# Kernel optimization log

Hardware: AMD Instinct MI355X
Metric: run time of the kernel (lower is better)

Reference implementation:

```python
import jax, jax.numpy as jnp
import numpy as np
from jax.ops import segment_sum

N_NODES = 100000
N_EDGES = 1600000
D = 128
N_LAYERS = 4
N_GRAPHS = 512
LN_EPS = 1e-5


def setup_inputs() -> dict:
    key = jax.random.key(0)
    ks = jax.random.split(key, 8)
    x = jax.random.normal(ks[0], (N_NODES, D), dtype=jnp.float32)
    edge_index = jax.random.randint(ks[1], (2, N_EDGES), 0, N_NODES, dtype=jnp.int64)
    batch = jnp.sort(jax.random.randint(ks[2], (N_NODES,), 0, N_GRAPHS, dtype=jnp.int64))
    scale = 1.0 / np.sqrt(D)
    Ws = jax.random.normal(ks[3], (N_LAYERS, D, D), dtype=jnp.float32) * scale
    bs = jnp.zeros((N_LAYERS, D), dtype=jnp.float32)
    gammas = jnp.ones((N_LAYERS, D), dtype=jnp.float32)
    betas = jnp.zeros((N_LAYERS, D), dtype=jnp.float32)
    lin_w = jax.random.normal(ks[4], (D, 1), dtype=jnp.float32) * scale
    lin_b = jnp.zeros((1,), dtype=jnp.float32)
    return {"x": x, "edge_index": edge_index, "batch": batch, "Ws": Ws,
            "bs": bs, "gammas": gammas, "betas": betas,
            "lin_w": lin_w, "lin_b": lin_b}


def _gcn_conv(x, W, b, src, dst, deg_inv_sqrt):
    # PyG GCNConv: h = x @ W, then sym-normalized aggregation over A + I, then + bias
    h = x @ W                                   # [N, D]
    coef = deg_inv_sqrt[src] * deg_inv_sqrt[dst]  # [E]
    msg = h[src] * coef[:, None]                # [E, D] gather (memory-bound)
    agg = segment_sum(msg, dst, num_segments=x.shape[0])  # scatter-add
    agg = agg + h * (deg_inv_sqrt * deg_inv_sqrt)[:, None]  # self-loop term
    return agg + b


def _layernorm(x, gamma, beta):
    mu = jnp.mean(x, axis=-1, keepdims=True)
    var = jnp.mean(jnp.square(x - mu), axis=-1, keepdims=True)
    return (x - mu) * jax.lax.rsqrt(var + LN_EPS) * gamma + beta


def reference(x, edge_index, batch, Ws, bs, gammas, betas, lin_w, lin_b):
    n = x.shape[0]
    src, dst = edge_index[0], edge_index[1]
    # degree with self-loops (GCNConv adds self loops by default)
    deg = segment_sum(jnp.ones_like(dst, dtype=x.dtype), dst, num_segments=n) + 1.0
    deg_inv_sqrt = jax.lax.rsqrt(deg)

    h = _gcn_conv(x, Ws[0], bs[0], src, dst, deg_inv_sqrt)
    h = _layernorm(h, gammas[0], betas[0])
    h = jax.nn.relu(h)  # dropout is identity in eval mode
    for i in range(1, N_LAYERS):
        h_prev = h
        h = _gcn_conv(h, Ws[i], bs[i], src, dst, deg_inv_sqrt)
        h = _layernorm(h, gammas[i], betas[i])
        h = h + h_prev
        if i < N_LAYERS - 1:
            h = jax.nn.relu(h)

    # global mean pool over graphs
    sums = segment_sum(h, batch, num_segments=N_GRAPHS)        # [G, D]
    cnts = segment_sum(jnp.ones((n,), h.dtype), batch, num_segments=N_GRAPHS)
    pooled = sums / jnp.maximum(cnts, 1.0)[:, None]
    return pooled @ lin_w + lin_b  # [G, 1]
```

## Files before the change

kernel.cpp:

```cpp
#include <hip/hip_runtime.h>
#include <hip/hip_bf16.h>


typedef __hip_bfloat162 bf2;
typedef __attribute__((ext_vector_type(8))) short short8;
typedef __attribute__((ext_vector_type(4))) float f32x4;

#define P1B 512
#define BSH 7
#define BMSK 127
#define MAXB 3072

__global__ __launch_bounds__(256) void k_pA(const int* __restrict__ dst,
                                            int* __restrict__ bh,
                                            const float* __restrict__ Ws,
                                            __hip_bfloat16* __restrict__ Wt,
                                            int* __restrict__ row_off,
                                            float* __restrict__ gsum,
                                            int E, int NB, int n, int G) {
    if (blockIdx.x >= P1B + 256) {
        for (int i = threadIdx.x; i < G; i += 256) gsum[i] = 0.f;
        if (threadIdx.x == 0) row_off[n] = E;
        return;
    }
    if (blockIdx.x >= P1B) {
        int i = (blockIdx.x - P1B) * 256 + threadIdx.x;
        int layer = i >> 14;
        int m = i & 16383;
        int j = m & 7;
        int l = (m >> 3) & 63;
        int ckb = m >> 9;
        int kb = ckb & 3;
        int c = ckb >> 2;
        int quad = l >> 4, lr = l & 15;
        int k = kb * 32 + quad * 8 + j;
        int col = c * 16 + lr;
        Wt[i] = __float2bfloat16(Ws[layer * 16384 + k * 128 + col]);
        return;
    }
    __shared__ int h[1024];
    const int tid = threadIdx.x;
    for (int i = tid; i < NB; i += 256) h[i] = 0;
    __syncthreads();
    const int per = (((E + P1B - 1) / P1B) + 3) & ~3;
    const int e0 = blockIdx.x * per, e1 = min(E, e0 + per);
    for (int base = e0 + tid * 4; base < e1; base += 1024) {
        if (base + 4 <= e1) {
            int4 d4 = *(const int4*)(dst + base);
            atomicAdd(&h[d4.x >> BSH], 1);
            atomicAdd(&h[d4.y >> BSH], 1);
            atomicAdd(&h[d4.z >> BSH], 1);
            atomicAdd(&h[d4.w >> BSH], 1);
        } else {
            for (int j = base; j < e1; j++) atomicAdd(&h[dst[j] >> BSH], 1);
        }
    }
    __syncthreads();
    int* out = bh + (size_t)blockIdx.x * NB;
    for (int i = tid; i < NB; i += 256) out[i] = h[i];
}

__global__ __launch_bounds__(256) void k_pB(int* __restrict__ bh,
                                            int* __restrict__ btot, int NB) {
    __shared__ int s[256];
    const int b = blockIdx.x, tid = threadIdx.x;
    int v0 = bh[(size_t)(2 * tid) * NB + b];
    int v1 = bh[(size_t)(2 * tid + 1) * NB + b];
    int tsum = v0 + v1;
    s[tid] = tsum;
    __syncthreads();
    for (int off = 1; off < 256; off <<= 1) {
        int t = (tid >= off) ? s[tid - off] : 0;
        __syncthreads();
        s[tid] += t;
        __syncthreads();
    }
    int excl = s[tid] - tsum;
    bh[(size_t)(2 * tid) * NB + b] = excl;
    bh[(size_t)(2 * tid + 1) * NB + b] = excl + v0;
    if (tid == 255) btot[b] = s[255];
}

__global__ __launch_bounds__(256) void k_pC(const int* __restrict__ src,
                                            const int* __restrict__ dst,
                                            const int* __restrict__ bh,
                                            const int* __restrict__ btot,
                                            int* __restrict__ bbase,
                                            unsigned* __restrict__ ebuf,
                                            int E, int NB) {
    __shared__ int cur[1024];
    __shared__ int s[256];
    const int tid = threadIdx.x;
    int v[4];
    int tsum = 0;
#pragma unroll
    for (int j = 0; j < 4; j++) {
        int idx = 4 * tid + j;
        v[j] = (idx < NB) ? btot[idx] : 0;
        tsum += v[j];
    }
    s[tid] = tsum;
    __syncthreads();
    for (int off = 1; off < 256; off <<= 1) {
        int t = (tid >= off) ? s[tid - off] : 0;
        __syncthreads();
        s[tid] += t;
        __syncthreads();
    }
    int excl = s[tid] - tsum;
#pragma unroll
    for (int j = 0; j < 4; j++) {
        int idx = 4 * tid + j;
        cur[idx] = excl;
        if (blockIdx.x == 0 && idx < NB) bbase[idx] = excl;
        excl += v[j];
    }
    __syncthreads();
    const int* cb = bh + (size_t)blockIdx.x * NB;
    for (int i = tid; i < NB; i += 256) cur[i] += cb[i];
    __syncthreads();
    const int per = (((E + P1B - 1) / P1B) + 3) & ~3;
    const int e0 = blockIdx.x * per, e1 = min(E, e0 + per);
    for (int base = e0 + tid * 4; base < e1; base += 1024) {
        if (base + 4 <= e1) {
            int4 d4 = *(const int4*)(dst + base);
            int4 s4 = *(const int4*)(src + base);
            int dd[4] = {d4.x, d4.y, d4.z, d4.w};
            int ss[4] = {s4.x, s4.y, s4.z, s4.w};
#pragma unroll
            for (int j = 0; j < 4; j++) {
                int p = atomicAdd(&cur[dd[j] >> BSH], 1);
                ebuf[p] = ((unsigned)(dd[j] & BMSK) << 17) | (unsigned)ss[j];
            }
        } else {
            for (int j = base; j < e1; j++) {
                int d = dst[j];
                int p = atomicAdd(&cur[d >> BSH], 1);
                ebuf[p] = ((unsigned)(d & BMSK) << 17) | (unsigned)src[j];
            }
        }
    }
}

__global__ __launch_bounds__(256) void k_pD(const unsigned* __restrict__ ebuf,
                                            const int* __restrict__ btot,
                                            const int* __restrict__ bbase,
                                            unsigned* __restrict__ colsrc,
                                            int* __restrict__ row_off,
                                            float* __restrict__ dis,
                                            const float* __restrict__ Xf,
                                            const __hip_bfloat16* __restrict__ Wt,
                                            __hip_bfloat16* __restrict__ Hb,
                                            int n, int NB) {
    __shared__ __align__(16) char smem[64 * 136 * 2];
    const int tid = threadIdx.x;
    if (blockIdx.x < (unsigned)NB) {
        unsigned* ein = (unsigned*)smem;
        int* hist = (int*)(smem + 12288);
        int* scn  = (int*)(smem + 12800);
        const int b = blockIdx.x;
        const int base = bbase[b];
        int sz = btot[b];
        if (sz > MAXB) sz = MAXB;
        if (tid < 128) hist[tid] = 0;
        __syncthreads();
        for (int i = tid; i < sz; i += 256) {
            unsigned v = ebuf[base + i];
            ein[i] = v;
            atomicAdd(&hist[v >> 17], 1);
        }
        __syncthreads();
        const int deg = (tid < 128) ? hist[tid] : 0;
        scn[tid] = deg;
        __syncthreads();
        for (int off = 1; off < 256; off <<= 1) {
            int t = (tid >= off) ? scn[tid - off] : 0;
            __syncthreads();
            scn[tid] += t;
            __syncthreads();
        }
        const int excl = scn[tid] - deg;
        const int node = b * 128 + tid;
        if (tid < 128 && node < n) {
            row_off[node] = base + excl;
            dis[node] = rsqrtf((float)deg + 1.0f);
        }
        if (tid < 128) hist[tid] = excl;
        __syncthreads();
        for (int i = tid; i < sz; i += 256) {
            unsigned v = ein[i];
            int p = atomicAdd(&hist[v >> 17], 1);
            colsrc[base + p] = v & 0x1FFFFu;
        }
        return;
    }
    __hip_bfloat16* sX = (__hip_bfloat16*)smem;
    const int row0 = (blockIdx.x - NB) * 64;
    for (int i = tid; i < 2048; i += 256) {
        int r = i >> 5, c = i & 31;
        int gr = row0 + r;
        float4 v = make_float4(0.f, 0.f, 0.f, 0.f);
        if (gr < n) v = *(const float4*)(Xf + (size_t)gr * 128 + c * 4);
        union { bf2 h2[2]; uint2 u; } pk;
        pk.h2[0].x = __float2bfloat16(v.x);
        pk.h2[0].y = __float2bfloat16(v.y);
        pk.h2[1].x = __float2bfloat16(v.z);
        pk.h2[1].y = __float2bfloat16(v.w);
        *(uint2*)(sX + r * 136 + c * 4) = pk.u;
    }
    __syncthreads();
    const int w = tid >> 6, l = tid & 63;
    const int quad = l >> 4, lr = l & 15;
    f32x4 acc[8];
#pragma unroll
    for (int c = 0; c < 8; c++) acc[c] = (f32x4){0.f, 0.f, 0.f, 0.f};
    short8 a[4];
#pragma unroll
    for (int kb = 0; kb < 4; kb++)
        a[kb] = *(const short8*)(sX + (w * 16 + lr) * 136 + kb * 32 + quad * 8);
#pragma unroll
    for (int c = 0; c < 8; c++) {
#pragma unroll
        for (int kb = 0; kb < 4; kb++) {
            short8 b = *(const short8*)(Wt + ((c * 4 + kb) * 64 + l) * 8);
            acc[c] = __builtin_amdgcn_mfma_f32_16x16x32_bf16(a[kb], b, acc[c], 0, 0, 0);
        }
    }
#pragma unroll
    for (int c = 0; c < 8; c++)
#pragma unroll
        for (int r = 0; r < 4; r++)
            sX[(w * 16 + quad * 4 + r) * 136 + c * 16 + lr] =
                __float2bfloat16(acc[c][r]);
#pragma unroll
    for (int p = 0; p < 4; p++) {
        int r = p * 4 + quad;
        int gr = row0 + w * 16 + r;
        uint4 v = *(const uint4*)(sX + (w * 16 + r) * 136 + lr * 8);
        if (gr < n) *(uint4*)(Hb + (size_t)gr * 128 + lr * 8) = v;
    }
}

__global__ __launch_bounds__(256) void k_matmul(const __hip_bfloat16* __restrict__ Xb,
                                                const __hip_bfloat16* __restrict__ Wt,
                                                __hip_bfloat16* __restrict__ Hb, int n) {
    __shared__ __align__(16) __hip_bfloat16 sX[64 * 136];
    const int tid = threadIdx.x;
    const int row0 = blockIdx.x * 64;
    for (int i = tid; i < 1024; i += 256) {
        int r = i >> 4, ck = i & 15;
        uint4 v = make_uint4(0, 0, 0, 0);
        int gr = row0 + r;
        if (gr < n) v = *(const uint4*)(Xb + (size_t)gr * 128 + ck * 8);
        *(uint4*)(sX + r * 136 + ck * 8) = v;
    }
    __syncthreads();
    const int w = tid >> 6, l = tid & 63;
    const int quad = l >> 4, lr = l & 15;
    f32x4 acc[8];
#pragma unroll
    for (int c = 0; c < 8; c++) acc[c] = (f32x4){0.f, 0.f, 0.f, 0.f};
    short8 a[4];
#pragma unroll
    for (int kb = 0; kb < 4; kb++)
        a[kb] = *(const short8*)(sX + (w * 16 + lr) * 136 + kb * 32 + quad * 8);
#pragma unroll
    for (int c = 0; c < 8; c++) {
#pragma unroll
        for (int kb = 0; kb < 4; kb++) {
            short8 b = *(const short8*)(Wt + ((c * 4 + kb) * 64 + l) * 8);
            acc[c] = __builtin_amdgcn_mfma_f32_16x16x32_bf16(a[kb], b, acc[c], 0, 0, 0);
        }
    }
#pragma unroll
    for (int c = 0; c < 8; c++)
#pragma unroll
        for (int r = 0; r < 4; r++)
            sX[(w * 16 + quad * 4 + r) * 136 + c * 16 + lr] =
                __float2bfloat16(acc[c][r]);
#pragma unroll
    for (int p = 0; p < 4; p++) {
        int r = p * 4 + quad;
        int gr = row0 + w * 16 + r;
        uint4 v = *(const uint4*)(sX + (w * 16 + r) * 136 + lr * 8);
        if (gr < n) *(uint4*)(Hb + (size_t)gr * 128 + lr * 8) = v;
    }
}

__global__ __launch_bounds__(256) void k_node(const __hip_bfloat16* __restrict__ Hb,
                                              __hip_bfloat16* __restrict__ Xb,
                                              const int* __restrict__ row_off,
                                              const unsigned* __restrict__ colsrc,
                                              const float* __restrict__ dis,
                                              const float* __restrict__ bias,
                                              const float* __restrict__ gamma,
                                              const float* __restrict__ beta,
                                              const float* __restrict__ lin_w,
                                              const int* __restrict__ batch,
                                              float* __restrict__ gsum,
                                              int do_relu, int do_res, int fuse_pool,
                                              int n) {
    __shared__ float spd[16];
    __shared__ int   sbt[16];
    const int wave = threadIdx.x >> 6;
    const int lane = threadIdx.x & 63;
    const int grp = lane >> 4;
    const int sub = lane & 15;
    const int node = blockIdx.x * 16 + wave * 4 + grp;
    const bool vn = node < n;
    const int nd = vn ? node : 0;
    const int e0 = vn ? row_off[node] : 0;
    const int e1 = vn ? row_off[node + 1] : 0;
    const char* hbase = (const char*)Hb;
    const unsigned suboff = (unsigned)(sub << 4);

    float dn = dis[nd];
    uint4 sv = *(const uint4*)(hbase + (((unsigned)nd) << 8) + suboff);

    float acc[8];
#pragma unroll
    for (int k = 0; k < 8; k++) acc[k] = 0.f;

    int e = e0;
    unsigned su[8];
#pragma unroll
    for (int u = 0; u < 8; u++) su[u] = colsrc[(e + u < e1) ? e + u : 0];

    while (__any(e < e1)) {
        uint4 v[8];
        float dv[8];
#pragma unroll
        for (int u = 0; u < 8; u++) {
            v[u] = *(const uint4*)(hbase + (su[u] << 8) + suboff);
            dv[u] = dis[su[u]];
        }
        const int en = e + 8;
        unsigned sn[8];
#pragma unroll
        for (int u = 0; u < 8; u++) sn[u] = colsrc[(en + u < e1) ? en + u : 0];
#pragma unroll
        for (int u = 0; u < 8; u++) {
            float c = (e + u < e1) ? dv[u] * dn : 0.f;
            acc[0] += __uint_as_float(v[u].x << 16) * c;
            acc[1] += __uint_as_float(v[u].x & 0xffff0000u) * c;
            acc[2] += __uint_as_float(v[u].y << 16) * c;
            acc[3] += __uint_as_float(v[u].y & 0xffff0000u) * c;
            acc[4] += __uint_as_float(v[u].z << 16) * c;
            acc[5] += __uint_as_float(v[u].z & 0xffff0000u) * c;
            acc[6] += __uint_as_float(v[u].w << 16) * c;
            acc[7] += __uint_as_float(v[u].w & 0xffff0000u) * c;
        }
#pragma unroll
        for (int u = 0; u < 8; u++) su[u] = sn[u];
        e = en;
    }

    {
        float dn2 = dn * dn;
        acc[0] += __uint_as_float(sv.x << 16) * dn2;
        acc[1] += __uint_as_float(sv.x & 0xffff0000u) * dn2;
        acc[2] += __uint_as_float(sv.y << 16) * dn2;
        acc[3] += __uint_as_float(sv.y & 0xffff0000u) * dn2;
        acc[4] += __uint_as_float(sv.z << 16) * dn2;
        acc[5] += __uint_as_float(sv.z & 0xffff0000u) * dn2;
        acc[6] += __uint_as_float(sv.w << 16) * dn2;
        acc[7] += __uint_as_float(sv.w & 0xffff0000u) * dn2;
    }
    float4 b0 = *(const float4*)(bias + sub * 8);
    float4 b1 = *(const float4*)(bias + sub * 8 + 4);
    acc[0] += b0.x; acc[1] += b0.y; acc[2] += b0.z; acc[3] += b0.w;
    acc[4] += b1.x; acc[5] += b1.y; acc[6] += b1.z; acc[7] += b1.w;

    float s = acc[0] + acc[1] + acc[2] + acc[3] + acc[4] + acc[5] + acc[6] + acc[7];
#pragma unroll
    for (int m = 8; m > 0; m >>= 1) s += __shfl_xor(s, m, 64);
    float mu = s * (1.f / 128.f);
    float vs = 0.f;
#pragma unroll
    for (int k = 0; k < 8; k++) {
        float d = acc[k] - mu;
        acc[k] = d;
        vs += d * d;
    }
#pragma unroll
    for (int m = 8; m > 0; m >>= 1) vs += __shfl_xor(vs, m, 64);
    float rs = rsqrtf(vs * (1.f / 128.f) + 1e-5f);

    float4 g0 = *(const float4*)(gamma + sub * 8);
    float4 g1 = *(const float4*)(gamma + sub * 8 + 4);
    float4 t0 = *(const float4*)(beta + sub * 8);
    float4 t1 = *(const float4*)(beta + sub * 8 + 4);
    float y[8];
    y[0] = acc[0] * rs * g0.x + t0.x;
    y[1] = acc[1] * rs * g0.y + t0.y;
    y[2] = acc[2] * rs * g0.z + t0.z;
    y[3] = acc[3] * rs * g0.w + t0.w;
    y[4] = acc[4] * rs * g1.x + t1.x;
    y[5] = acc[5] * rs * g1.y + t1.y;
    y[6] = acc[6] * rs * g1.z + t1.z;
    y[7] = acc[7] * rs * g1.w + t1.w;

    __hip_bfloat16* xp = Xb + (size_t)node * 128 + sub * 8;
    if (vn && do_res) {
        uint4 rv = *(const uint4*)xp;
        y[0] += __uint_as_float(rv.x << 16);
        y[1] += __uint_as_float(rv.x & 0xffff0000u);
        y[2] += __uint_as_float(rv.y << 16);
        y[3] += __uint_as_float(rv.y & 0xffff0000u);
        y[4] += __uint_as_float(rv.z << 16);
        y[5] += __uint_as_float(rv.z & 0xffff0000u);
        y[6] += __uint_as_float(rv.w << 16);
        y[7] += __uint_as_float(rv.w & 0xffff0000u);
    }

    if (fuse_pool) {
        float4 w0 = *(const float4*)(lin_w + sub * 8);
        float4 w1 = *(const float4*)(lin_w + sub * 8 + 4);
        float pdot = y[0] * w0.x + y[1] * w0.y + y[2] * w0.z + y[3] * w0.w +
                     y[4] * w1.x + y[5] * w1.y + y[6] * w1.z + y[7] * w1.w;
#pragma unroll
        for (int m = 8; m > 0; m >>= 1) pdot += __shfl_xor(pdot, m, 64);
        int slot = wave * 4 + grp;
        if (sub == 0) {
            spd[slot] = vn ? pdot : 0.f;
            sbt[slot] = vn ? batch[node] : -1;
        }
        __syncthreads();
        if (threadIdx.x == 0) {
            int i = 0;
            while (i < 16) {
                int b = sbt[i];
                if (b < 0) { i++; continue; }
                float acc2 = spd[i];
                int j = i + 1;
                while (j < 16 && sbt[j] == b) { acc2 += spd[j]; j++; }
                atomicAdd(&gsum[b], acc2);
                i = j;
            }
        }
    } else if (vn) {
        if (do_relu) {
#pragma unroll
            for (int k = 0; k < 8; k++) y[k] = fmaxf(y[k], 0.f);
        }
        union { bf2 h2[4]; uint4 u; } pk;
        pk.h2[0].x = __float2bfloat16(y[0]); pk.h2[0].y = __float2bfloat16(y[1]);
        pk.h2[1].x = __float2bfloat16(y[2]); pk.h2[1].y = __float2bfloat16(y[3]);
        pk.h2[2].x = __float2bfloat16(y[4]); pk.h2[2].y = __float2bfloat16(y[5]);
        pk.h2[3].x = __float2bfloat16(y[6]); pk.h2[3].y = __float2bfloat16(y[7]);
        *(uint4*)xp = pk.u;
    }
}

__global__ void k_out(const float* __restrict__ gsum, const int* __restrict__ batch,
                      const float* __restrict__ lin_b, float* __restrict__ out,
                      int n, int G) {
    int g = blockIdx.x * blockDim.x + threadIdx.x;
    if (g >= G) return;
    int lo = 0, hi = n;
    while (lo < hi) { int m = (lo + hi) >> 1; if (batch[m] < g) lo = m + 1; else hi = m; }
    int start = lo;
    hi = n;
    while (lo < hi) { int m = (lo + hi) >> 1; if (batch[m] <= g) lo = m + 1; else hi = m; }
    float c = (float)(lo - start);
    out[g] = gsum[g] / fmaxf(c, 1.f) + lin_b[0];
}

extern "C" void kernel_launch(void* const* d_in, const int* in_sizes, int n_in,
                              void* d_out, int out_size, void* d_ws, size_t ws_size,
                              hipStream_t stream) {
    const float* x      = (const float*)d_in[0];
    const int*   eidx   = (const int*)d_in[1];
    const int*   batch  = (const int*)d_in[2];
    const float* Ws     = (const float*)d_in[3];
    const float* bs     = (const float*)d_in[4];
    const float* gammas = (const float*)d_in[5];
    const float* betas  = (const float*)d_in[6];
    const float* lin_w  = (const float*)d_in[7];
    const float* lin_b  = (const float*)d_in[8];
    float* out = (float*)d_out;

    const int n = in_sizes[2];
    const int E = in_sizes[1] / 2;
    const int G = out_size;
    const int NB = (n + BMSK) >> BSH;

    const int* src  = eidx;
    const int* dstp = eidx + E;

    char* w = (char*)d_ws;
    size_t off = 0;
    auto alloc = [&](size_t bytes) {
        void* p = w + off;
        off = (off + bytes + 15) & ~(size_t)15;
        return p;
    };
    int*      bh      = (int*)     alloc((size_t)P1B * NB * 4);
    int*      btot    = (int*)     alloc((size_t)NB * 4);
    int*      bbase   = (int*)     alloc((size_t)NB * 4);
    unsigned* ebuf    = (unsigned*)alloc((size_t)E * 4);
    unsigned* colsrc  = (unsigned*)alloc((size_t)E * 4);
    int*      row_off = (int*)     alloc((size_t)(n + 1) * 4);
    float*    dis     = (float*)   alloc((size_t)n * 4);
    float*    gsum    = (float*)   alloc((size_t)G * 4);
    __hip_bfloat16* hb = (__hip_bfloat16*)alloc((size_t)n * 128 * 2);
    __hip_bfloat16* xb = (__hip_bfloat16*)alloc((size_t)n * 128 * 2);
    __hip_bfloat16* wt = (__hip_bfloat16*)alloc((size_t)4 * 128 * 128 * 2);
    (void)ws_size; (void)n_in;

    const int mm_tiles = (n + 63) / 64;

    k_pA<<<P1B + 256 + 1, 256, 0, stream>>>(dstp, bh, Ws, wt, row_off, gsum,
                                            E, NB, n, G);
    k_pB<<<NB, 256, 0, stream>>>(bh, btot, NB);
    k_pC<<<P1B, 256, 0, stream>>>(src, dstp, bh, btot, bbase, ebuf, E, NB);
    k_pD<<<NB + mm_tiles, 256, 0, stream>>>(ebuf, btot, bbase, colsrc,
                                            row_off, dis, x, wt, hb, n, NB);

    for (int layer = 0; layer < 4; layer++) {
        if (layer > 0)
            k_matmul<<<mm_tiles, 256, 0, stream>>>(xb, wt + (size_t)layer * 16384,
                                                   hb, n);
        k_node<<<(n + 15) / 16, 256, 0, stream>>>(hb, xb, row_off, colsrc, dis,
                                                  bs + (size_t)layer * 128,
                                                  gammas + (size_t)layer * 128,
                                                  betas + (size_t)layer * 128,
                                                  lin_w, batch, gsum,
                                                  (layer < 3) ? 1 : 0, (layer > 0) ? 1 : 0,
                                                  (layer == 3) ? 1 : 0, n);
    }
    k_out<<<(G + 255) / 256, 256, 0, stream>>>(gsum, batch, lin_b, out, n, G);
}
```

Baseline: 550.9 us.

## Replace two-pass bucket histogram sort with single-pass global-atomic fixed slabs

```diff
diff --git a/kernel.cpp b/kernel.cpp
--- a/kernel.cpp
+++ b/kernel.cpp
@@ -6,25 +6,18 @@
 typedef __attribute__((ext_vector_type(8))) short short8;
 typedef __attribute__((ext_vector_type(4))) float f32x4;
 
-#define P1B 512
 #define BSH 7
 #define BMSK 127
 #define MAXB 3072
 
-__global__ __launch_bounds__(256) void k_pA(const int* __restrict__ dst,
-                                            int* __restrict__ bh,
-                                            const float* __restrict__ Ws,
+__global__ __launch_bounds__(256) void k_pW(const float* __restrict__ Ws,
                                             __hip_bfloat16* __restrict__ Wt,
+                                            int* __restrict__ bcnt,
+                                            float* __restrict__ gsum,
                                             int* __restrict__ row_off,
-                                            float* __restrict__ gsum,
                                             int E, int NB, int n, int G) {
-    if (blockIdx.x >= P1B + 256) {
-        for (int i = threadIdx.x; i < G; i += 256) gsum[i] = 0.f;
-        if (threadIdx.x == 0) row_off[n] = E;
-        return;
-    }
-    if (blockIdx.x >= P1B) {
-        int i = (blockIdx.x - P1B) * 256 + threadIdx.x;
+    if (blockIdx.x < 256) {
+        int i = blockIdx.x * 256 + threadIdx.x;
         int layer = i >> 14;
         int m = i & 16383;
         int j = m & 7;
@@ -38,35 +31,56 @@
         Wt[i] = __float2bfloat16(Ws[layer * 16384 + k * 128 + col]);
         return;
     }
-    __shared__ int h[1024];
+    if (blockIdx.x == 256) {
+        for (int i = threadIdx.x; i < G; i += 256) gsum[i] = 0.f;
+        if (threadIdx.x == 0) row_off[n] = E;
+        return;
+    }
+    for (int i = threadIdx.x; i < NB; i += 256) bcnt[i] = 0;
+}
+
+__global__ __launch_bounds__(256) void k_pC2(const int* __restrict__ src,
+                                             const int* __restrict__ dst,
+                                             int* __restrict__ bcnt,
+                                             unsigned* __restrict__ ebuf, int E) {
+    int base = (blockIdx.x * 256 + threadIdx.x) * 4;
+    if (base + 4 <= E) {
+        int4 d4 = *(const int4*)(dst + base);
+        int4 s4 = *(const int4*)(src + base);
+        int dd[4] = {d4.x, d4.y, d4.z, d4.w};
+        int ss[4] = {s4.x, s4.y, s4.z, s4.w};
+#pragma unroll
+        for (int j = 0; j < 4; j++) {
+            int b = dd[j] >> BSH;
+            int p = atomicAdd(&bcnt[b], 1);
+            if (p < MAXB)
+                ebuf[(size_t)b * MAXB + p] =
+                    ((unsigned)(dd[j] & BMSK) << 17) | (unsigned)ss[j];
+        }
+    } else {
+        for (int j = base; j < E; j++) {
+            int d = dst[j];
+            int b = d >> BSH;
+            int p = atomicAdd(&bcnt[b], 1);
+            if (p < MAXB)
+                ebuf[(size_t)b * MAXB + p] =
+                    ((unsigned)(d & BMSK) << 17) | (unsigned)src[j];
+        }
+    }
+}
+
+__global__ __launch_bounds__(256) void k_pS(const int* __restrict__ bcnt,
+                                            int* __restrict__ bbase, int NB) {
+    __shared__ int s[256];
     const int tid = threadIdx.x;
-    for (int i = tid; i < NB; i += 256) h[i] = 0;
-    __syncthreads();
-    const int per = (((E + P1B - 1) / P1B) + 3) & ~3;
-    const int e0 = blockIdx.x * per, e1 = min(E, e0 + per);
-    for (int base = e0 + tid * 4; base < e1; base += 1024) {
-        if (base + 4 <= e1) {
-            int4 d4 = *(const int4*)(dst + base);
-            atomicAdd(&h[d4.x >> BSH], 1);
-            atomicAdd(&h[d4.y >> BSH], 1);
-            atomicAdd(&h[d4.z >> BSH], 1);
-            atomicAdd(&h[d4.w >> BSH], 1);
-        } else {
-            for (int j = base; j < e1; j++) atomicAdd(&h[dst[j] >> BSH], 1);
-        }
-    }
-    __syncthreads();
-    int* out = bh + (size_t)blockIdx.x * NB;
-    for (int i = tid; i < NB; i += 256) out[i] = h[i];
-}
-
-__global__ __launch_bounds__(256) void k_pB(int* __restrict__ bh,
-                                            int* __restrict__ btot, int NB) {
-    __shared__ int s[256];
-    const int b = blockIdx.x, tid = threadIdx.x;
-    int v0 = bh[(size_t)(2 * tid) * NB + b];
-    int v1 = bh[(size_t)(2 * tid + 1) * NB + b];
-    int tsum = v0 + v1;
+    int v[4];
+    int tsum = 0;
+#pragma unroll
+    for (int j = 0; j < 4; j++) {
+        int idx = 4 * tid + j;
+        v[j] = (idx < NB) ? min(bcnt[idx], MAXB) : 0;
+        tsum += v[j];
+    }
     s[tid] = tsum;
     __syncthreads();
     for (int off = 1; off < 256; off <<= 1) {
@@ -76,82 +90,24 @@
         __syncthreads();
     }
     int excl = s[tid] - tsum;
-    bh[(size_t)(2 * tid) * NB + b] = excl;
-    bh[(size_t)(2 * tid + 1) * NB + b] = excl + v0;
-    if (tid == 255) btot[b] = s[255];
-}
-
-__global__ __launch_bounds__(256) void k_pC(const int* __restrict__ src,
-                                            const int* __restrict__ dst,
-                                            const int* __restrict__ bh,
-                                            const int* __restrict__ btot,
-                                            int* __restrict__ bbase,
-                                            unsigned* __restrict__ ebuf,
-                                            int E, int NB) {
-    __shared__ int cur[1024];
-    __shared__ int s[256];
-    const int tid = threadIdx.x;
-    int v[4];
-    int tsum = 0;
 #pragma unroll
     for (int j = 0; j < 4; j++) {
         int idx = 4 * tid + j;
-        v[j] = (idx < NB) ? btot[idx] : 0;
-        tsum += v[j];
-    }
-    s[tid] = tsum;
-    __syncthreads();
-    for (int off = 1; off < 256; off <<= 1) {
-        int t = (tid >= off) ? s[tid - off] : 0;
-        __syncthreads();
-        s[tid] += t;
-        __syncthreads();
-    }
-    int excl = s[tid] - tsum;
-#pragma unroll
-    for (int j = 0; j < 4; j++) {
-        int idx = 4 * tid + j;
-        cur[idx] = excl;
-        if (blockIdx.x == 0 && idx < NB) bbase[idx] = excl;
+        if (idx < NB) bbase[idx] = excl;
         excl += v[j];
     }
-    __syncthreads();
-    const int* cb = bh + (size_t)blockIdx.x * NB;
-    for (int i = tid; i < NB; i += 256) cur[i] += cb[i];
-    __syncthreads();
-    const int per = (((E + P1B - 1) / P1B) + 3) & ~3;
-    const int e0 = blockIdx.x * per, e1 = min(E, e0 + per);
-    for (int base = e0 + tid * 4; base < e1; base += 1024) {
-        if (base + 4 <= e1) {
-            int4 d4 = *(const int4*)(dst + base);
-            int4 s4 = *(const int4*)(src + base);
-            int dd[4] = {d4.x, d4.y, d4.z, d4.w};
-            int ss[4] = {s4.x, s4.y, s4.z, s4.w};
-#pragma unroll
-            for (int j = 0; j < 4; j++) {
-                int p = atomicAdd(&cur[dd[j] >> BSH], 1);
-                ebuf[p] = ((unsigned)(dd[j] & BMSK) << 17) | (unsigned)ss[j];
-            }
-        } else {
-            for (int j = base; j < e1; j++) {
-                int d = dst[j];
-                int p = atomicAdd(&cur[d >> BSH], 1);
-                ebuf[p] = ((unsigned)(d & BMSK) << 17) | (unsigned)src[j];
-            }
-        }
-    }
-}
-
-__global__ __launch_bounds__(256) void k_pD(const unsigned* __restrict__ ebuf,
-                                            const int* __restrict__ btot,
-                                            const int* __restrict__ bbase,
-                                            unsigned* __restrict__ colsrc,
-                                            int* __restrict__ row_off,
-                                            float* __restrict__ dis,
-                                            const float* __restrict__ Xf,
-                                            const __hip_bfloat16* __restrict__ Wt,
-                                            __hip_bfloat16* __restrict__ Hb,
-                                            int n, int NB) {
+}
+
+__global__ __launch_bounds__(256) void k_pD2(const unsigned* __restrict__ ebuf,
+                                             const int* __restrict__ bcnt,
+                                             const int* __restrict__ bbase,
+                                             unsigned* __restrict__ colsrc,
+                                             int* __restrict__ row_off,
+                                             float* __restrict__ dis,
+                                             const float* __restrict__ Xf,
+                                             const __hip_bfloat16* __restrict__ Wt,
+                                             __hip_bfloat16* __restrict__ Hb,
+                                             int n, int NB) {
     __shared__ __align__(16) char smem[64 * 136 * 2];
     const int tid = threadIdx.x;
     if (blockIdx.x < (unsigned)NB) {
@@ -160,12 +116,13 @@
         int* scn  = (int*)(smem + 12800);
         const int b = blockIdx.x;
         const int base = bbase[b];
-        int sz = btot[b];
+        const size_t slab = (size_t)b * MAXB;
+        int sz = bcnt[b];
         if (sz > MAXB) sz = MAXB;
         if (tid < 128) hist[tid] = 0;
         __syncthreads();
         for (int i = tid; i < sz; i += 256) {
-            unsigned v = ebuf[base + i];
+            unsigned v = ebuf[slab + i];
             ein[i] = v;
             atomicAdd(&hist[v >> 17], 1);
         }
@@ -495,10 +452,9 @@
         off = (off + bytes + 15) & ~(size_t)15;
         return p;
     };
-    int*      bh      = (int*)     alloc((size_t)P1B * NB * 4);
-    int*      btot    = (int*)     alloc((size_t)NB * 4);
+    int*      bcnt    = (int*)     alloc((size_t)NB * 4);
     int*      bbase   = (int*)     alloc((size_t)NB * 4);
-    unsigned* ebuf    = (unsigned*)alloc((size_t)E * 4);
+    unsigned* ebuf    = (unsigned*)alloc((size_t)NB * MAXB * 4);
     unsigned* colsrc  = (unsigned*)alloc((size_t)E * 4);
     int*      row_off = (int*)     alloc((size_t)(n + 1) * 4);
     float*    dis     = (float*)   alloc((size_t)n * 4);
@@ -510,12 +466,11 @@
 
     const int mm_tiles = (n + 63) / 64;
 
-    k_pA<<<P1B + 256 + 1, 256, 0, stream>>>(dstp, bh, Ws, wt, row_off, gsum,
-                                            E, NB, n, G);
-    k_pB<<<NB, 256, 0, stream>>>(bh, btot, NB);
-    k_pC<<<P1B, 256, 0, stream>>>(src, dstp, bh, btot, bbase, ebuf, E, NB);
-    k_pD<<<NB + mm_tiles, 256, 0, stream>>>(ebuf, btot, bbase, colsrc,
-                                            row_off, dis, x, wt, hb, n, NB);
+    k_pW<<<258, 256, 0, stream>>>(Ws, wt, bcnt, gsum, row_off, E, NB, n, G);
+    k_pC2<<<(E + 1023) / 1024, 256, 0, stream>>>(src, dstp, bcnt, ebuf, E);
+    k_pS<<<1, 256, 0, stream>>>(bcnt, bbase, NB);
+    k_pD2<<<NB + mm_tiles, 256, 0, stream>>>(ebuf, bcnt, bbase, colsrc,
+                                             row_off, dis, x, wt, hb, n, NB);
 
     for (int layer = 0; layer < 4; layer++) {
         if (layer > 0)
```

Result: slower. 905.1 us (+64.3%).
